# Kernel tuning notes

Hardware: AMD Instinct MI355X
Metric: run time of the kernel (lower is better)

The kernel has to match this reference:

```python
import jax, jax.numpy as jnp
import numpy as np

N_LAYER, N_HEAD, D_PARAM = 4, 8, 63
BATCH, SEQ, D_FULL = 16, 2048, D_PARAM + 1
VAR = 0.02


def setup_inputs() -> dict:
    key = jax.random.key(0)
    kz, kp = jax.random.split(key)
    Z = jax.random.normal(kz, (BATCH, SEQ, D_FULL), dtype=jnp.float32)
    allparam = VAR * jax.random.normal(kp, (N_LAYER, N_HEAD, 2, D_PARAM, D_PARAM), dtype=jnp.float32)
    return {"Z": Z, "allparam": allparam}


def _augment(P, Q, d_full):
    # P_full: P in top-left block, bottom-right corner = 1, rest zeros.
    dp = P.shape[0]
    P_full = jnp.zeros((d_full, d_full), P.dtype).at[:dp, :dp].set(P).at[dp, dp].set(1.0)
    # Q_full: Q in top-left block, rest zeros (bottom-right corner stays 0).
    Q_full = jnp.zeros((d_full, d_full), Q.dtype).at[:dp, :dp].set(Q)
    return P_full, Q_full


def _attention(P, Q, Z):
    B, N, d = Z.shape
    P_full, Q_full = _augment(P, Q, d)
    # attn[b,n,m] = Z[b,n,:] @ Q_full @ Z[b,m,:]
    attn = jnp.einsum('BNi,ij,BMj->BNM', Z, Q_full, Z)
    key = jnp.einsum('ij,BNj->BNi', P_full, Z)
    # A = eye(N) with A[N-1,N-1] = 0  => zero out last token of key before aggregation.
    key = key.at[:, N - 1, :].set(0.0)
    out = jnp.einsum('BNM,BMi->BNi', attn, key)
    return out / (N - 1)


def reference(Z, allparam):
    n_layer, n_head = allparam.shape[0], allparam.shape[1]
    for i in range(n_layer):
        Zi = Z
        residues = jnp.zeros_like(Z)
        for j in range(n_head):
            residues = residues + _attention(allparam[i, j, 0], allparam[i, j, 1], Zi)
        Z = Zi + residues
    return Z
```

## Files before the change

kernel.cpp:

```cpp
#include <hip/hip_runtime.h>

constexpr int NH = 8, DP = 63, D = 64, BATCH = 16, S = 2048;
constexpr float INVS = 1.0f / 2047.0f;
constexpr int NBLK = 128;

__device__ __forceinline__ void gsync(unsigned int* bar, unsigned int target) {
    __syncthreads();
    if (threadIdx.x == 0) {
        __builtin_amdgcn_fence(__ATOMIC_RELEASE, "agent");
        __hip_atomic_fetch_add(bar, 1u, __ATOMIC_RELAXED, __HIP_MEMORY_SCOPE_AGENT);
        while (__hip_atomic_load(bar, __ATOMIC_RELAXED, __HIP_MEMORY_SCOPE_AGENT) < target)
            __builtin_amdgcn_s_sleep(2);
        __builtin_amdgcn_fence(__ATOMIC_ACQUIRE, "agent");
    }
    __syncthreads();
}

__global__ __launch_bounds__(256) void fused_all(
    const float* __restrict__ Z, const float* __restrict__ params,
    float* __restrict__ out, float* __restrict__ Gp, float* __restrict__ H,
    unsigned int* bar) {
    __shared__ float4 sm4[5120];
    float* As = (float*)sm4;
    float* Ms = (float*)(sm4 + 1024);
    float* Pt = (float*)(sm4 + 2048);
    float* Qt = (float*)(sm4 + 3072);
    float* Tb = (float*)(sm4 + 4096);
    const int bid = blockIdx.x, t = threadIdx.x;
    const int b = bid >> 3, j = bid & 7;
    unsigned int tgt = NBLK;

    {
        float* ZN = (float*)(sm4 + 3072);
        const int w = t >> 6, l = t & 63, qy = l >> 3, rx = l & 7;
        float g[8][8];
#pragma unroll
        for (int a = 0; a < 8; ++a)
#pragma unroll
            for (int bb = 0; bb < 8; ++bb) g[a][bb] = 0.f;

        for (int half = 0; half < 2; ++half) {
            const int rowbase = j * 256 + half * 128;
#pragma unroll
            for (int k = 0; k < 8; ++k) {
                const int row = (t >> 4) + 16 * k, c4 = t & 15;
                const int grow = rowbase + row;
                float4 v = *(const float4*)&Z[((size_t)b * S + grow) * D + 4 * c4];
                if (grow == S - 1) v = make_float4(0.f, 0.f, 0.f, 0.f);
                *(float4*)&ZN[row * 64 + 4 * (c4 ^ ((row >> 3) & 15))] = v;
            }
            __syncthreads();
#pragma unroll 4
            for (int mi = 0; mi < 32; ++mi) {
                const int m = 32 * w + mi;
                const int f = (m >> 3) & 15;
                const float* rowp = &ZN[m * 64];
                float4 a0 = *(const float4*)&rowp[4 * (qy ^ f)];
                float4 a1 = *(const float4*)&rowp[4 * ((qy + 8) ^ f)];
                float4 b0 = *(const float4*)&rowp[4 * (rx ^ f)];
                float4 b1 = *(const float4*)&rowp[4 * ((rx + 8) ^ f)];
                float A[8]  = {a0.x, a0.y, a0.z, a0.w, a1.x, a1.y, a1.z, a1.w};
                float Bv[8] = {b0.x, b0.y, b0.z, b0.w, b1.x, b1.y, b1.z, b1.w};
#pragma unroll
                for (int a = 0; a < 8; ++a)
#pragma unroll
                    for (int bb = 0; bb < 8; ++bb) g[a][bb] += A[a] * Bv[bb];
            }
            __syncthreads();
        }
        float* part = (float*)(sm4 + w * 1024);
#pragma unroll
        for (int a = 0; a < 8; ++a) {
            const int q = 4 * qy + (a & 3) + 32 * (a >> 2);
            *(float4*)&part[q * 64 + 4 * rx]      = make_float4(g[a][0], g[a][1], g[a][2], g[a][3]);
            *(float4*)&part[q * 64 + 32 + 4 * rx] = make_float4(g[a][4], g[a][5], g[a][6], g[a][7]);
        }
        __syncthreads();
        float4* gp4 = (float4*)(Gp + (size_t)(b * 8 + j) * 4096);
#pragma unroll
        for (int k = 0; k < 4; ++k) {
            const int e4 = t + 256 * k;
            float4 s0 = sm4[e4], s1 = sm4[1024 + e4], s2 = sm4[2048 + e4], s3 = sm4[3072 + e4];
            gp4[e4] = make_float4(s0.x + s1.x + s2.x + s3.x, s0.y + s1.y + s2.y + s3.y,
                                  s0.z + s1.z + s2.z + s3.z, s0.w + s1.w + s2.w + s3.w);
        }
    }
    gsync(bar, tgt); tgt += NBLK;

    {
        const float4* Gp4 = (const float4*)Gp;
        float4* As4 = (float4*)As; float4* Ms4 = (float4*)Ms;
#pragma unroll
        for (int k = 0; k < 4; ++k) {
            const int e4 = t + 256 * k;
            float4 sum = make_float4(0.f, 0.f, 0.f, 0.f);
            for (int p = 0; p < 8; ++p) {
                float4 gg = Gp4[(size_t)(b * 8 + p) * 1024 + e4];
                sum.x += gg.x; sum.y += gg.y; sum.z += gg.z; sum.w += gg.w;
            }
            As4[e4] = sum;
            float iv[4];
#pragma unroll
            for (int c = 0; c < 4; ++c) {
                const int e = 4 * e4 + c;
                iv[c] = ((e >> 6) == (e & 63)) ? 1.f : 0.f;
            }
            Ms4[e4] = make_float4(iv[0], iv[1], iv[2], iv[3]);
        }
    }

    for (int layer = 0; layer < 4; ++layer) {
        float* Hl = H + (size_t)(layer & 1) * ((size_t)BATCH * NH * 4096);
        const float* P = params + ((size_t)(layer * NH + j) * 2) * (DP * DP);
        const float* Q = P + DP * DP;
        {
            const int rr = t & 63, qtr = t >> 6;
#pragma unroll
            for (int k = 0; k < 16; ++k) {
                const int i = qtr * 16 + k;
                float pv = 0.f;
                if (rr < DP && i < DP) pv = P[(size_t)i * DP + rr];
                else if (rr == DP && i == DP) pv = 1.f;
                Pt[rr * 64 + 4 * ((i >> 2) ^ (rr & 15)) + (i & 3)] = pv;
                const float qv = (i < DP && rr < DP) ? Q[(size_t)i * DP + rr] : 0.f;
                Qt[rr * 64 + 4 * ((i >> 2) ^ (rr & 15)) + (i & 3)] = qv;
            }
        }
        __syncthreads();
        const int ty = t >> 4, tx = t & 15;
        {
            float acc[4][4] = {};
#pragma unroll 4
            for (int r = 0; r < 64; ++r) {
                float4 av = *(const float4*)&As[r * 64 + 4 * ty];
                float4 bv = *(const float4*)&Pt[r * 64 + 4 * (tx ^ (r & 15))];
                float A[4] = {av.x, av.y, av.z, av.w}, Bb[4] = {bv.x, bv.y, bv.z, bv.w};
#pragma unroll
                for (int a = 0; a < 4; ++a)
#pragma unroll
                    for (int c = 0; c < 4; ++c) acc[a][c] += A[a] * Bb[c];
            }
#pragma unroll
            for (int a = 0; a < 4; ++a)
                *(float4*)&Tb[(4 * ty + a) * 64 + 4 * tx] =
                    make_float4(acc[a][0], acc[a][1], acc[a][2], acc[a][3]);
        }
        __syncthreads();
        {
            float acc2[4][4] = {};
#pragma unroll 4
            for (int q = 0; q < 64; ++q) {
                float4 av = *(const float4*)&Qt[q * 64 + 4 * (ty ^ (q & 15))];
                float4 bv = *(const float4*)&Tb[q * 64 + 4 * tx];
                float A[4] = {av.x, av.y, av.z, av.w}, Bb[4] = {bv.x, bv.y, bv.z, bv.w};
#pragma unroll
                for (int a = 0; a < 4; ++a)
#pragma unroll
                    for (int c = 0; c < 4; ++c) acc2[a][c] += A[a] * Bb[c];
            }
            float* Hb = Hl + (size_t)(b * NH + j) * 4096;
#pragma unroll
            for (int a = 0; a < 4; ++a)
                *(float4*)&Hb[(4 * ty + a) * 64 + 4 * tx] =
                    make_float4(acc2[a][0] * INVS, acc2[a][1] * INVS,
                                acc2[a][2] * INVS, acc2[a][3] * INVS);
        }
        gsync(bar, tgt); tgt += NBLK;

        {
            float4* Ws4 = (float4*)Pt;
            const float4* H4 = (const float4*)Hl;
#pragma unroll
            for (int k = 0; k < 4; ++k) {
                const int e4 = t + 256 * k;
                float iv[4];
#pragma unroll
                for (int c = 0; c < 4; ++c) {
                    const int e = 4 * e4 + c;
                    iv[c] = ((e >> 6) == (e & 63)) ? 1.f : 0.f;
                }
                float4 w = make_float4(iv[0], iv[1], iv[2], iv[3]);
                for (int jj = 0; jj < 8; ++jj) {
                    float4 h = H4[(size_t)(b * 8 + jj) * 1024 + e4];
                    w.x += h.x; w.y += h.y; w.z += h.z; w.w += h.w;
                }
                Ws4[e4] = w;
            }
        }
        __syncthreads();
        float* Ws = Pt;
        if (layer < 3) {
            {
                float acc[4][4] = {};
#pragma unroll 4
                for (int r = 0; r < 64; ++r) {
                    float4 av = *(const float4*)&As[r * 64 + 4 * ty];
                    float4 bv = *(const float4*)&Ws[r * 64 + 4 * tx];
                    float A[4] = {av.x, av.y, av.z, av.w}, Bb[4] = {bv.x, bv.y, bv.z, bv.w};
#pragma unroll
                    for (int a = 0; a < 4; ++a)
#pragma unroll
                        for (int c = 0; c < 4; ++c) acc[a][c] += A[a] * Bb[c];
                }
#pragma unroll
                for (int a = 0; a < 4; ++a)
                    *(float4*)&Tb[(4 * ty + a) * 64 + 4 * tx] =
                        make_float4(acc[a][0], acc[a][1], acc[a][2], acc[a][3]);
            }
            __syncthreads();
            float accG[4][4] = {}, accM[4][4] = {};
#pragma unroll 4
            for (int p = 0; p < 64; ++p) {
                float4 av = *(const float4*)&Ws[p * 64 + 4 * ty];
                float4 bv = *(const float4*)&Tb[p * 64 + 4 * tx];
                float4 cv = *(const float4*)&Ms[p * 64 + 4 * tx];
                float A[4] = {av.x, av.y, av.z, av.w};
                float Bb[4] = {bv.x, bv.y, bv.z, bv.w};
                float Cc[4] = {cv.x, cv.y, cv.z, cv.w};
#pragma unroll
                for (int a = 0; a < 4; ++a)
#pragma unroll
                    for (int c = 0; c < 4; ++c) {
                        accG[a][c] += A[a] * Bb[c];
                        accM[a][c] += A[a] * Cc[c];
                    }
            }
            __syncthreads();
#pragma unroll
            for (int a = 0; a < 4; ++a) {
                *(float4*)&As[(4 * ty + a) * 64 + 4 * tx] =
                    make_float4(accG[a][0], accG[a][1], accG[a][2], accG[a][3]);
                *(float4*)&Ms[(4 * ty + a) * 64 + 4 * tx] =
                    make_float4(accM[a][0], accM[a][1], accM[a][2], accM[a][3]);
            }
            __syncthreads();
        } else {
            float accM[4][4] = {};
#pragma unroll 4
            for (int p = 0; p < 64; ++p) {
                float4 av = *(const float4*)&Ms[p * 64 + 4 * ty];
                float4 bv = *(const float4*)&Ws[p * 64 + 4 * tx];
                float A[4] = {av.x, av.y, av.z, av.w}, Bb[4] = {bv.x, bv.y, bv.z, bv.w};
#pragma unroll
                for (int a = 0; a < 4; ++a)
#pragma unroll
                    for (int c = 0; c < 4; ++c) accM[a][c] += A[a] * Bb[c];
            }
            __syncthreads();
#pragma unroll
            for (int a = 0; a < 4; ++a)
                *(float4*)&Tb[(4 * ty + a) * 64 + 4 * tx] =
                    make_float4(accM[a][0], accM[a][1], accM[a][2], accM[a][3]);
            __syncthreads();
        }
    }

    {
        float* ZT = (float*)sm4;
        float* Ws = Tb;
        const int ny = t & 15, ix = t >> 4;
        for (int half = 0; half < 2; ++half) {
            const size_t zbase = ((size_t)b * S + j * 256 + half * 128) * D;
            __syncthreads();
#pragma unroll
            for (int k = 0; k < 8; ++k) {
                const int row = (t >> 4) + 16 * k, c4 = t & 15;
                float4 v = *(const float4*)&Z[zbase + (size_t)row * D + 4 * c4];
                float vv[4] = {v.x, v.y, v.z, v.w};
#pragma unroll
                for (int c = 0; c < 4; ++c)
                    ZT[(4 * c4 + c) * 128 + 4 * ((row >> 2) ^ c4) + (row & 3)] = vv[c];
            }
            __syncthreads();
            float acc[8][4] = {};
#pragma unroll 4
            for (int p = 0; p < 64; ++p) {
                const int f = p >> 2;
                const float* zp = &ZT[p * 128];
                float4 a0 = *(const float4*)&zp[4 * (ny ^ f)];
                float4 a1 = *(const float4*)&zp[4 * ((ny + 16) ^ f)];
                float4 wv = *(const float4*)&Ws[p * 64 + 4 * ix];
                float A[8] = {a0.x, a0.y, a0.z, a0.w, a1.x, a1.y, a1.z, a1.w};
                float Wv[4] = {wv.x, wv.y, wv.z, wv.w};
#pragma unroll
                for (int a = 0; a < 8; ++a)
#pragma unroll
                    for (int c = 0; c < 4; ++c) acc[a][c] += A[a] * Wv[c];
            }
#pragma unroll
            for (int a = 0; a < 8; ++a) {
                const int n = 4 * ny + (a & 3) + 64 * (a >> 2);
                *(float4*)&out[zbase + (size_t)n * D + 4 * ix] =
                    make_float4(acc[a][0], acc[a][1], acc[a][2], acc[a][3]);
            }
        }
    }
}

extern "C" void kernel_launch(void* const* d_in, const int* in_sizes, int n_in,
                              void* d_out, int out_size, void* d_ws, size_t ws_size,
                              hipStream_t stream) {
    const float* Z        = (const float*)d_in[0];
    const float* allparam = (const float*)d_in[1];
    float* out = (float*)d_out;

    float* Gp = (float*)d_ws;
    float* H  = Gp + (size_t)NBLK * 4096;
    unsigned int* bar = (unsigned int*)(H + 2 * (size_t)BATCH * NH * 4096);

    hipMemsetAsync(bar, 0, 64, stream);
    fused_all<<<NBLK, 256, 0, stream>>>(Z, allparam, out, Gp, H, bar);
}
```

Baseline: 221.6 us.

## Double grid to 256 blocks and use hierarchical grid barrier

```diff
diff --git a/kernel.cpp b/kernel.cpp
--- a/kernel.cpp
+++ b/kernel.cpp
@@ -2,14 +2,21 @@
 
 constexpr int NH = 8, DP = 63, D = 64, BATCH = 16, S = 2048;
 constexpr float INVS = 1.0f / 2047.0f;
-constexpr int NBLK = 128;
-
-__device__ __forceinline__ void gsync(unsigned int* bar, unsigned int target) {
+constexpr int NBLK = 256;
+constexpr int NGRP = 16, GRPSZ = 16;
+
+__device__ __forceinline__ void gsync(unsigned int* bar, int grp, unsigned int r) {
     __syncthreads();
     if (threadIdx.x == 0) {
+        unsigned int* grpc = bar + 32u * (1u + (unsigned)grp);
+        unsigned int* root = bar;
         __builtin_amdgcn_fence(__ATOMIC_RELEASE, "agent");
-        __hip_atomic_fetch_add(bar, 1u, __ATOMIC_RELAXED, __HIP_MEMORY_SCOPE_AGENT);
-        while (__hip_atomic_load(bar, __ATOMIC_RELAXED, __HIP_MEMORY_SCOPE_AGENT) < target)
+        unsigned int old = __hip_atomic_fetch_add(grpc, 1u, __ATOMIC_RELAXED,
+                                                  __HIP_MEMORY_SCOPE_AGENT);
+        if (old == (unsigned)(GRPSZ * r - 1))
+            __hip_atomic_fetch_add(root, 1u, __ATOMIC_RELAXED, __HIP_MEMORY_SCOPE_AGENT);
+        while (__hip_atomic_load(root, __ATOMIC_RELAXED, __HIP_MEMORY_SCOPE_AGENT)
+               < (unsigned)(NGRP * r))
             __builtin_amdgcn_s_sleep(2);
         __builtin_amdgcn_fence(__ATOMIC_ACQUIRE, "agent");
     }
@@ -27,8 +34,8 @@
     float* Qt = (float*)(sm4 + 3072);
     float* Tb = (float*)(sm4 + 4096);
     const int bid = blockIdx.x, t = threadIdx.x;
-    const int b = bid >> 3, j = bid & 7;
-    unsigned int tgt = NBLK;
+    const int b = bid >> 4, u = bid & 15;
+    unsigned int r = 1;
 
     {
         float* ZN = (float*)(sm4 + 3072);
@@ -39,35 +46,33 @@
 #pragma unroll
             for (int bb = 0; bb < 8; ++bb) g[a][bb] = 0.f;
 
-        for (int half = 0; half < 2; ++half) {
-            const int rowbase = j * 256 + half * 128;
-#pragma unroll
-            for (int k = 0; k < 8; ++k) {
-                const int row = (t >> 4) + 16 * k, c4 = t & 15;
-                const int grow = rowbase + row;
-                float4 v = *(const float4*)&Z[((size_t)b * S + grow) * D + 4 * c4];
-                if (grow == S - 1) v = make_float4(0.f, 0.f, 0.f, 0.f);
-                *(float4*)&ZN[row * 64 + 4 * (c4 ^ ((row >> 3) & 15))] = v;
-            }
-            __syncthreads();
-#pragma unroll 4
-            for (int mi = 0; mi < 32; ++mi) {
-                const int m = 32 * w + mi;
-                const int f = (m >> 3) & 15;
-                const float* rowp = &ZN[m * 64];
-                float4 a0 = *(const float4*)&rowp[4 * (qy ^ f)];
-                float4 a1 = *(const float4*)&rowp[4 * ((qy + 8) ^ f)];
-                float4 b0 = *(const float4*)&rowp[4 * (rx ^ f)];
-                float4 b1 = *(const float4*)&rowp[4 * ((rx + 8) ^ f)];
-                float A[8]  = {a0.x, a0.y, a0.z, a0.w, a1.x, a1.y, a1.z, a1.w};
-                float Bv[8] = {b0.x, b0.y, b0.z, b0.w, b1.x, b1.y, b1.z, b1.w};
-#pragma unroll
-                for (int a = 0; a < 8; ++a)
-#pragma unroll
-                    for (int bb = 0; bb < 8; ++bb) g[a][bb] += A[a] * Bv[bb];
-            }
-            __syncthreads();
-        }
+        const int rowbase = u * 128;
+#pragma unroll
+        for (int k = 0; k < 8; ++k) {
+            const int row = (t >> 4) + 16 * k, c4 = t & 15;
+            const int grow = rowbase + row;
+            float4 v = *(const float4*)&Z[((size_t)b * S + grow) * D + 4 * c4];
+            if (grow == S - 1) v = make_float4(0.f, 0.f, 0.f, 0.f);
+            *(float4*)&ZN[row * 64 + 4 * (c4 ^ ((row >> 3) & 15))] = v;
+        }
+        __syncthreads();
+#pragma unroll 4
+        for (int mi = 0; mi < 32; ++mi) {
+            const int m = 32 * w + mi;
+            const int f = (m >> 3) & 15;
+            const float* rowp = &ZN[m * 64];
+            float4 a0 = *(const float4*)&rowp[4 * (qy ^ f)];
+            float4 a1 = *(const float4*)&rowp[4 * ((qy + 8) ^ f)];
+            float4 b0 = *(const float4*)&rowp[4 * (rx ^ f)];
+            float4 b1 = *(const float4*)&rowp[4 * ((rx + 8) ^ f)];
+            float A[8]  = {a0.x, a0.y, a0.z, a0.w, a1.x, a1.y, a1.z, a1.w};
+            float Bv[8] = {b0.x, b0.y, b0.z, b0.w, b1.x, b1.y, b1.z, b1.w};
+#pragma unroll
+            for (int a = 0; a < 8; ++a)
+#pragma unroll
+                for (int bb = 0; bb < 8; ++bb) g[a][bb] += A[a] * Bv[bb];
+        }
+        __syncthreads();
         float* part = (float*)(sm4 + w * 1024);
 #pragma unroll
         for (int a = 0; a < 8; ++a) {
@@ -76,7 +81,7 @@
             *(float4*)&part[q * 64 + 32 + 4 * rx] = make_float4(g[a][4], g[a][5], g[a][6], g[a][7]);
         }
         __syncthreads();
-        float4* gp4 = (float4*)(Gp + (size_t)(b * 8 + j) * 4096);
+        float4* gp4 = (float4*)(Gp + (size_t)(b * 16 + u) * 4096);
 #pragma unroll
         for (int k = 0; k < 4; ++k) {
             const int e4 = t + 256 * k;
@@ -85,7 +90,7 @@
                                   s0.z + s1.z + s2.z + s3.z, s0.w + s1.w + s2.w + s3.w);
         }
     }
-    gsync(bar, tgt); tgt += NBLK;
+    gsync(bar, b, r); ++r;
 
     {
         const float4* Gp4 = (const float4*)Gp;
@@ -94,8 +99,8 @@
         for (int k = 0; k < 4; ++k) {
             const int e4 = t + 256 * k;
             float4 sum = make_float4(0.f, 0.f, 0.f, 0.f);
-            for (int p = 0; p < 8; ++p) {
-                float4 gg = Gp4[(size_t)(b * 8 + p) * 1024 + e4];
+            for (int p = 0; p < 16; ++p) {
+                float4 gg = Gp4[(size_t)(b * 16 + p) * 1024 + e4];
                 sum.x += gg.x; sum.y += gg.y; sum.z += gg.z; sum.w += gg.w;
             }
             As4[e4] = sum;
@@ -111,61 +116,64 @@
 
     for (int layer = 0; layer < 4; ++layer) {
         float* Hl = H + (size_t)(layer & 1) * ((size_t)BATCH * NH * 4096);
-        const float* P = params + ((size_t)(layer * NH + j) * 2) * (DP * DP);
-        const float* Q = P + DP * DP;
-        {
-            const int rr = t & 63, qtr = t >> 6;
-#pragma unroll
-            for (int k = 0; k < 16; ++k) {
-                const int i = qtr * 16 + k;
-                float pv = 0.f;
-                if (rr < DP && i < DP) pv = P[(size_t)i * DP + rr];
-                else if (rr == DP && i == DP) pv = 1.f;
-                Pt[rr * 64 + 4 * ((i >> 2) ^ (rr & 15)) + (i & 3)] = pv;
-                const float qv = (i < DP && rr < DP) ? Q[(size_t)i * DP + rr] : 0.f;
-                Qt[rr * 64 + 4 * ((i >> 2) ^ (rr & 15)) + (i & 3)] = qv;
-            }
-        }
-        __syncthreads();
         const int ty = t >> 4, tx = t & 15;
-        {
-            float acc[4][4] = {};
-#pragma unroll 4
-            for (int r = 0; r < 64; ++r) {
-                float4 av = *(const float4*)&As[r * 64 + 4 * ty];
-                float4 bv = *(const float4*)&Pt[r * 64 + 4 * (tx ^ (r & 15))];
-                float A[4] = {av.x, av.y, av.z, av.w}, Bb[4] = {bv.x, bv.y, bv.z, bv.w};
-#pragma unroll
-                for (int a = 0; a < 4; ++a)
-#pragma unroll
-                    for (int c = 0; c < 4; ++c) acc[a][c] += A[a] * Bb[c];
-            }
-#pragma unroll
-            for (int a = 0; a < 4; ++a)
-                *(float4*)&Tb[(4 * ty + a) * 64 + 4 * tx] =
-                    make_float4(acc[a][0], acc[a][1], acc[a][2], acc[a][3]);
-        }
-        __syncthreads();
-        {
-            float acc2[4][4] = {};
-#pragma unroll 4
-            for (int q = 0; q < 64; ++q) {
-                float4 av = *(const float4*)&Qt[q * 64 + 4 * (ty ^ (q & 15))];
-                float4 bv = *(const float4*)&Tb[q * 64 + 4 * tx];
-                float A[4] = {av.x, av.y, av.z, av.w}, Bb[4] = {bv.x, bv.y, bv.z, bv.w};
-#pragma unroll
-                for (int a = 0; a < 4; ++a)
-#pragma unroll
-                    for (int c = 0; c < 4; ++c) acc2[a][c] += A[a] * Bb[c];
-            }
-            float* Hb = Hl + (size_t)(b * NH + j) * 4096;
-#pragma unroll
-            for (int a = 0; a < 4; ++a)
-                *(float4*)&Hb[(4 * ty + a) * 64 + 4 * tx] =
-                    make_float4(acc2[a][0] * INVS, acc2[a][1] * INVS,
-                                acc2[a][2] * INVS, acc2[a][3] * INVS);
-        }
-        gsync(bar, tgt); tgt += NBLK;
+        if (u < NH) {
+            const int j = u;
+            const float* P = params + ((size_t)(layer * NH + j) * 2) * (DP * DP);
+            const float* Q = P + DP * DP;
+            {
+                const int rr = t & 63, qtr = t >> 6;
+#pragma unroll
+                for (int k = 0; k < 16; ++k) {
+                    const int i = qtr * 16 + k;
+                    float pv = 0.f;
+                    if (rr < DP && i < DP) pv = P[(size_t)i * DP + rr];
+                    else if (rr == DP && i == DP) pv = 1.f;
+                    Pt[rr * 64 + 4 * ((i >> 2) ^ (rr & 15)) + (i & 3)] = pv;
+                    const float qv = (i < DP && rr < DP) ? Q[(size_t)i * DP + rr] : 0.f;
+                    Qt[rr * 64 + 4 * ((i >> 2) ^ (rr & 15)) + (i & 3)] = qv;
+                }
+            }
+            __syncthreads();
+            {
+                float acc[4][4] = {};
+#pragma unroll 4
+                for (int rr = 0; rr < 64; ++rr) {
+                    float4 av = *(const float4*)&As[rr * 64 + 4 * ty];
+                    float4 bv = *(const float4*)&Pt[rr * 64 + 4 * (tx ^ (rr & 15))];
+                    float A[4] = {av.x, av.y, av.z, av.w}, Bb[4] = {bv.x, bv.y, bv.z, bv.w};
+#pragma unroll
+                    for (int a = 0; a < 4; ++a)
+#pragma unroll
+                        for (int c = 0; c < 4; ++c) acc[a][c] += A[a] * Bb[c];
+                }
+#pragma unroll
+                for (int a = 0; a < 4; ++a)
+                    *(float4*)&Tb[(4 * ty + a) * 64 + 4 * tx] =
+                        make_float4(acc[a][0], acc[a][1], acc[a][2], acc[a][3]);
+            }
+            __syncthreads();
+            {
+                float acc2[4][4] = {};
+#pragma unroll 4
+                for (int q = 0; q < 64; ++q) {
+                    float4 av = *(const float4*)&Qt[q * 64 + 4 * (ty ^ (q & 15))];
+                    float4 bv = *(const float4*)&Tb[q * 64 + 4 * tx];
+                    float A[4] = {av.x, av.y, av.z, av.w}, Bb[4] = {bv.x, bv.y, bv.z, bv.w};
+#pragma unroll
+                    for (int a = 0; a < 4; ++a)
+#pragma unroll
+                        for (int c = 0; c < 4; ++c) acc2[a][c] += A[a] * Bb[c];
+                }
+                float* Hb = Hl + (size_t)(b * NH + j) * 4096;
+#pragma unroll
+                for (int a = 0; a < 4; ++a)
+                    *(float4*)&Hb[(4 * ty + a) * 64 + 4 * tx] =
+                        make_float4(acc2[a][0] * INVS, acc2[a][1] * INVS,
+                                    acc2[a][2] * INVS, acc2[a][3] * INVS);
+            }
+        }
+        gsync(bar, b, r); ++r;
 
         {
             float4* Ws4 = (float4*)Pt;
@@ -188,14 +196,14 @@
             }
         }
         __syncthreads();
-        float* Ws = Pt;
+        const float* Ws = Pt;
         if (layer < 3) {
             {
                 float acc[4][4] = {};
 #pragma unroll 4
-                for (int r = 0; r < 64; ++r) {
-                    float4 av = *(const float4*)&As[r * 64 + 4 * ty];
-                    float4 bv = *(const float4*)&Ws[r * 64 + 4 * tx];
+                for (int rr = 0; rr < 64; ++rr) {
+                    float4 av = *(const float4*)&As[rr * 64 + 4 * ty];
+                    float4 bv = *(const float4*)&Ws[rr * 64 + 4 * tx];
                     float A[4] = {av.x, av.y, av.z, av.w}, Bb[4] = {bv.x, bv.y, bv.z, bv.w};
 #pragma unroll
                     for (int a = 0; a < 4; ++a)
@@ -257,42 +265,39 @@
 
     {
         float* ZT = (float*)sm4;
-        float* Ws = Tb;
+        const float* Ws = Tb;
         const int ny = t & 15, ix = t >> 4;
-        for (int half = 0; half < 2; ++half) {
-            const size_t zbase = ((size_t)b * S + j * 256 + half * 128) * D;
-            __syncthreads();
-#pragma unroll
-            for (int k = 0; k < 8; ++k) {
-                const int row = (t >> 4) + 16 * k, c4 = t & 15;
-                float4 v = *(const float4*)&Z[zbase + (size_t)row * D + 4 * c4];
-                float vv[4] = {v.x, v.y, v.z, v.w};
-#pragma unroll
-                for (int c = 0; c < 4; ++c)
-                    ZT[(4 * c4 + c) * 128 + 4 * ((row >> 2) ^ c4) + (row & 3)] = vv[c];
-            }
-            __syncthreads();
-            float acc[8][4] = {};
-#pragma unroll 4
-            for (int p = 0; p < 64; ++p) {
-                const int f = p >> 2;
-                const float* zp = &ZT[p * 128];
-                float4 a0 = *(const float4*)&zp[4 * (ny ^ f)];
-                float4 a1 = *(const float4*)&zp[4 * ((ny + 16) ^ f)];
-                float4 wv = *(const float4*)&Ws[p * 64 + 4 * ix];
-                float A[8] = {a0.x, a0.y, a0.z, a0.w, a1.x, a1.y, a1.z, a1.w};
-                float Wv[4] = {wv.x, wv.y, wv.z, wv.w};
-#pragma unroll
-                for (int a = 0; a < 8; ++a)
-#pragma unroll
-                    for (int c = 0; c < 4; ++c) acc[a][c] += A[a] * Wv[c];
-            }
-#pragma unroll
-            for (int a = 0; a < 8; ++a) {
-                const int n = 4 * ny + (a & 3) + 64 * (a >> 2);
-                *(float4*)&out[zbase + (size_t)n * D + 4 * ix] =
-                    make_float4(acc[a][0], acc[a][1], acc[a][2], acc[a][3]);
-            }
+        const size_t zbase = ((size_t)b * S + u * 128) * D;
+#pragma unroll
+        for (int k = 0; k < 8; ++k) {
+            const int row = (t >> 4) + 16 * k, c4 = t & 15;
+            float4 v = *(const float4*)&Z[zbase + (size_t)row * D + 4 * c4];
+            float vv[4] = {v.x, v.y, v.z, v.w};
+#pragma unroll
+            for (int c = 0; c < 4; ++c)
+                ZT[(4 * c4 + c) * 128 + 4 * ((row >> 2) ^ c4) + (row & 3)] = vv[c];
+        }
+        __syncthreads();
+        float acc[8][4] = {};
+#pragma unroll 4
+        for (int p = 0; p < 64; ++p) {
+            const int f = p >> 2;
+            const float* zp = &ZT[p * 128];
+            float4 a0 = *(const float4*)&zp[4 * (ny ^ f)];
+            float4 a1 = *(const float4*)&zp[4 * ((ny + 16) ^ f)];
+            float4 wv = *(const float4*)&Ws[p * 64 + 4 * ix];
+            float A[8] = {a0.x, a0.y, a0.z, a0.w, a1.x, a1.y, a1.z, a1.w};
+            float Wv[4] = {wv.x, wv.y, wv.z, wv.w};
+#pragma unroll
+            for (int a = 0; a < 8; ++a)
+#pragma unroll
+                for (int c = 0; c < 4; ++c) acc[a][c] += A[a] * Wv[c];
+        }
+#pragma unroll
+        for (int a = 0; a < 8; ++a) {
+            const int n = 4 * ny + (a & 3) + 64 * (a >> 2);
+            *(float4*)&out[zbase + (size_t)n * D + 4 * ix] =
+                make_float4(acc[a][0], acc[a][1], acc[a][2], acc[a][3]);
         }
     }
 }
@@ -308,6 +313,6 @@
     float* H  = Gp + (size_t)NBLK * 4096;
     unsigned int* bar = (unsigned int*)(H + 2 * (size_t)BATCH * NH * 4096);
 
-    hipMemsetAsync(bar, 0, 64, stream);
+    hipMemsetAsync(bar, 0, 4096, stream);
     fused_all<<<NBLK, 256, 0, stream>>>(Z, allparam, out, Gp, H, bar);
 }
```

Result: no change. 220.9 us (-0.3%).
